# Kernel tuning notes

Measured on AMD Instinct MI355X. Metric: run time of the kernel, lower is better.

Reference implementation:

```python
import jax, jax.numpy as jnp
import numpy as np

SCALE = 32 ** (-0.5)  # hardcoded in the original module, independent of head_size

def setup_inputs() -> dict:
    key = jax.random.key(0)
    k1, k2, k3, k4 = jax.random.split(key, 4)
    B, T, E, H = 8, 4096, 2048, 128
    x = jax.random.normal(k1, (B, T, E), dtype=jnp.float32)
    Wq = jax.random.normal(k2, (E, H), dtype=jnp.float32) * (E ** -0.5)
    Wk = jax.random.normal(k3, (E, H), dtype=jnp.float32) * (E ** -0.5)
    Wv = jax.random.normal(k4, (E, H), dtype=jnp.float32) * (E ** -0.5)
    return {"x": x, "Wq": Wq, "Wk": Wk, "Wv": Wv}

def reference(x, Wq, Wk, Wv):
    # q,k,v: [B,T,H]
    q = jnp.einsum('bte,eh->bth', x, Wq)
    k = jnp.einsum('bte,eh->bth', x, Wk)
    v = jnp.einsum('bte,eh->bth', x, Wv)
    # wei: [B, T(query), T(key)]
    wei = jnp.einsum('bqh,bkh->bqk', q, k) * SCALE
    # NOTE: original uses F.softmax(wei, dim=1) -> normalize over the QUERY axis
    wei = jax.nn.softmax(wei, axis=1)
    # dropout prob is 0 in this deterministic baseline (eval mode)
    out = jnp.einsum('bqk,bkh->bqh', wei, v)
    return out
```

## Files before the change

kernel.cpp:

```cpp
#include <hip/hip_runtime.h>
#include <hip/hip_bf16.h>
#include <hip/hip_fp16.h>

#define Bn 8
#define Tn 4096
#define En 2048
#define Hn 128

typedef __attribute__((ext_vector_type(8))) short bf16x8;
typedef __attribute__((ext_vector_type(4))) float f32x4;
typedef __attribute__((ext_vector_type(4))) unsigned int u32x4;

typedef const __attribute__((address_space(1))) unsigned int* gptr_t;
typedef __attribute__((address_space(3))) unsigned int* lptr_t;

static __device__ __forceinline__ void gload16(const void* g, void* l) {
    __builtin_amdgcn_global_load_lds((gptr_t)g, (lptr_t)l, 16, 0, 0);
}

static __device__ __forceinline__ unsigned short f2bf(float f) {
    union { float f; unsigned u; } v; v.f = f;
    unsigned r = v.u + 0x7FFFu + ((v.u >> 16) & 1u);
    return (unsigned short)(r >> 16);
}

#define MFMA16(a, b, c) __builtin_amdgcn_mfma_f32_16x16x32_bf16((a), (b), (c), 0, 0, 0)
#define EXP2F(x) __builtin_amdgcn_exp2f(x)
#define WAIT_VM_PUB(N) do { asm volatile("s_waitcnt vmcnt(" #N ")" ::: "memory"); \
                            __builtin_amdgcn_sched_barrier(0); \
                            __builtin_amdgcn_s_barrier(); \
                            __builtin_amdgcn_sched_barrier(0); } while (0)
#define LGKM_BARRIER() do { asm volatile("s_waitcnt lgkmcnt(0)" ::: "memory"); \
                            __builtin_amdgcn_s_barrier(); \
                            __builtin_amdgcn_sched_barrier(0); } while (0)

__global__ __launch_bounds__(256) void conv_x(const float* __restrict__ x,
                                              unsigned short* __restrict__ xb) {
    size_t i = ((size_t)blockIdx.x * 256 + threadIdx.x) * 8;
    float4 a = *reinterpret_cast<const float4*>(x + i);
    float4 b = *reinterpret_cast<const float4*>(x + i + 4);
    ushort4 o0, o1;
    o0.x = f2bf(a.x); o0.y = f2bf(a.y); o0.z = f2bf(a.z); o0.w = f2bf(a.w);
    o1.x = f2bf(b.x); o1.y = f2bf(b.y); o1.z = f2bf(b.z); o1.w = f2bf(b.w);
    *reinterpret_cast<ushort4*>(xb + i) = o0;
    *reinterpret_cast<ushort4*>(xb + i + 4) = o1;
}

__global__ __launch_bounds__(256) void prep_w(const float* __restrict__ Wq,
                                              const float* __restrict__ Wk,
                                              const float* __restrict__ Wv,
                                              unsigned short* __restrict__ Wt) {
    int idx = blockIdx.x * 256 + threadIdx.x;
    int w = idx / (En * Hn);
    int rem = idx - w * (En * Hn);
    int kx = rem >> 7;
    int n  = rem & 127;
    const float* W = (w == 0) ? Wq : (w == 1) ? Wk : Wv;
    float f = W[rem];
    if (w == 0) f *= (0.17677669529663687f * 1.4426950408889634f);
    Wt[(size_t)w * En * Hn + (size_t)n * En + kx] = f2bf(f);
}

__global__ __launch_bounds__(256, 3) void qkv_mfma(const unsigned short* __restrict__ xb,
                                                   const unsigned short* __restrict__ Wt,
                                                   unsigned short* __restrict__ qs,
                                                   unsigned short* __restrict__ ks,
                                                   unsigned short* __restrict__ vT) {
    __shared__ unsigned short Al[128][64];
    __shared__ unsigned short Bl[128][64];
    const int bid = blockIdx.x;
    const int w = bid % 3;
    const int m0 = (bid / 3) * 128;
    const int b = m0 >> 12;
    const int tb = m0 & (Tn - 1);
    const int t = threadIdx.x;
    const int lane = t & 63, wid = t >> 6;
    const int wr = (wid >> 1) * 64, wc = (wid & 1) * 64;
    const int fr = lane & 15, fq = lane >> 4;
    const unsigned short* Wb = Wt + (size_t)w * En * Hn;
    const int sr = lane >> 3, sc = lane & 7;

    f32x4 acc[4][4] = {};
    for (int k0 = 0; k0 < En; k0 += 64) {
        __syncthreads();
        #pragma unroll
        for (int s = 0; s < 4; ++s) {
            int seg = wid * 4 + s;
            int r = seg * 8 + sr;
            gload16(&xb[(size_t)(m0 + r) * En + k0 + sc * 8],
                    (char*)&Al[0][0] + seg * 1024 + lane * 16);
            gload16(&Wb[(size_t)r * En + k0 + sc * 8],
                    (char*)&Bl[0][0] + seg * 1024 + lane * 16);
        }
        __syncthreads();
        #pragma unroll
        for (int ksub = 0; ksub < 2; ++ksub) {
            bf16x8 av[4], bv[4];
            #pragma unroll
            for (int mi = 0; mi < 4; ++mi)
                av[mi] = *reinterpret_cast<const bf16x8*>(&Al[wr + mi * 16 + fr][ksub * 32 + fq * 8]);
            #pragma unroll
            for (int ni = 0; ni < 4; ++ni)
                bv[ni] = *reinterpret_cast<const bf16x8*>(&Bl[wc + ni * 16 + fr][ksub * 32 + fq * 8]);
            #pragma unroll
            for (int mi = 0; mi < 4; ++mi)
                #pragma unroll
                for (int ni = 0; ni < 4; ++ni)
                    acc[mi][ni] = MFMA16(av[mi], bv[ni], acc[mi][ni]);
        }
    }

    if (w < 2) {
        unsigned short* out = (w == 0) ? qs : ks;
        #pragma unroll
        for (int mi = 0; mi < 4; ++mi)
            #pragma unroll
            for (int ni = 0; ni < 4; ++ni)
                #pragma unroll
                for (int r = 0; r < 4; ++r) {
                    int row = m0 + wr + mi * 16 + fq * 4 + r;
                    int col = wc + ni * 16 + fr;
                    out[(size_t)row * Hn + col] = f2bf(acc[mi][ni][r]);
                }
    } else {
        #pragma unroll
        for (int mi = 0; mi < 4; ++mi)
            #pragma unroll
            for (int ni = 0; ni < 4; ++ni)
                #pragma unroll
                for (int r = 0; r < 4; ++r) {
                    int tt = tb + wr + mi * 16 + fq * 4 + r;
                    int h  = wc + ni * 16 + fr;
                    vT[((size_t)b * Hn + h) * Tn + tt] = f2bf(acc[mi][ni][r]);
                }
    }
}

__global__ __launch_bounds__(256, 3) void stats_qk(const unsigned short* __restrict__ qs,
                                                   const unsigned short* __restrict__ ks,
                                                   float2* __restrict__ part) {
    __shared__ __align__(16) char smem[49152];
    const int bid = blockIdx.x;
    const int b = bid >> 7;
    const int kt = (bid >> 1) & 63;
    const int qh = bid & 1;
    const int k0 = kt * 64;
    const unsigned short* qb = qs + (size_t)b * Tn * Hn;
    const unsigned short* kb = ks + (size_t)b * Tn * Hn;
    const int t = threadIdx.x;
    const int lane = t & 63, wid = t >> 6;
    const int wk = wid >> 1, wq = wid & 1;
    const int fr = lane & 15, fq = lane >> 4;
    const int srow = t >> 4, schk = t & 15;

    #pragma unroll
    for (int it = 0; it < 4; ++it) {
        int r = it * 16 + srow;
        gload16(&kb[(size_t)(k0 + r) * Hn + ((schk ^ (r & 15)) * 8)],
                smem + it * 4096 + t * 16);
        gload16(&qb[(size_t)(qh * 2048 + r) * Hn + ((schk ^ (r & 15)) * 8)],
                smem + 16384 + it * 4096 + t * 16);
    }
    __syncthreads();
    bf16x8 av[2][4];
    #pragma unroll
    for (int mi = 0; mi < 2; ++mi)
        #pragma unroll
        for (int kc = 0; kc < 4; ++kc) {
            int row = wk * 32 + mi * 16 + fr;
            int ch = (kc * 4 + fq) ^ (row & 15);
            av[mi][kc] = *reinterpret_cast<const bf16x8*>(smem + row * 256 + ch * 16);
        }

    float m[2][4], l[2][4];
    #pragma unroll
    for (int mi = 0; mi < 2; ++mi)
        #pragma unroll
        for (int r = 0; r < 4; ++r) { m[mi][r] = -INFINITY; l[mi][r] = 0.f; }

    for (int step = 0; step < 32; ++step) {
        const int cur = step & 1;
        const int qn = qh * 2048 + ((step + 1) & 31) * 64;
        #pragma unroll
        for (int it = 0; it < 4; ++it) {
            int r = it * 16 + srow;
            gload16(&qb[(size_t)(qn + r) * Hn + ((schk ^ (r & 15)) * 8)],
                    smem + 16384 + (cur ^ 1) * 16384 + it * 4096 + t * 16);
        }
        WAIT_VM_PUB(4);
        const char* Qc = smem + 16384 + cur * 16384;
        f32x4 acc[2][2] = {};
        __builtin_amdgcn_s_setprio(1);
        #pragma unroll
        for (int kc = 0; kc < 4; ++kc) {
            bf16x8 bv[2];
            #pragma unroll
            for (int ni = 0; ni < 2; ++ni) {
                int row = wq * 32 + ni * 16 + fr;
                int ch = (kc * 4 + fq) ^ (row & 15);
                bv[ni] = *reinterpret_cast<const bf16x8*>(Qc + row * 256 + ch * 16);
            }
            #pragma unroll
            for (int mi = 0; mi < 2; ++mi)
                #pragma unroll
                for (int ni = 0; ni < 2; ++ni)
                    acc[mi][ni] = MFMA16(av[mi][kc], bv[ni], acc[mi][ni]);
        }
        __builtin_amdgcn_s_setprio(0);
        #pragma unroll
        for (int mi = 0; mi < 2; ++mi)
            #pragma unroll
            for (int r = 0; r < 4; ++r) {
                float v0 = acc[mi][0][r], v1 = acc[mi][1][r];
                float mn = fmaxf(m[mi][r], fmaxf(v0, v1));
                l[mi][r] = l[mi][r] * EXP2F(m[mi][r] - mn) + EXP2F(v0 - mn) + EXP2F(v1 - mn);
                m[mi][r] = mn;
            }
        LGKM_BARRIER();
    }
    #pragma unroll
    for (int off = 1; off <= 8; off <<= 1) {
        #pragma unroll
        for (int mi = 0; mi < 2; ++mi)
            #pragma unroll
            for (int r = 0; r < 4; ++r) {
                float mo = __shfl_xor(m[mi][r], off);
                float lo = __shfl_xor(l[mi][r], off);
                float mn = fmaxf(m[mi][r], mo);
                l[mi][r] = l[mi][r] * EXP2F(m[mi][r] - mn) + lo * EXP2F(mo - mn);
                m[mi][r] = mn;
            }
    }
    if (fr == 0) {
        #pragma unroll
        for (int mi = 0; mi < 2; ++mi)
            #pragma unroll
            for (int r = 0; r < 4; ++r) {
                int k = k0 + wk * 32 + mi * 16 + fq * 4 + r;
                part[((size_t)b * Tn + k) * 4 + qh * 2 + wq] = make_float2(m[mi][r], l[mi][r]);
            }
    }
}

__global__ __launch_bounds__(256) void stats_comb(const float2* __restrict__ part,
                                                  float* __restrict__ mr) {
    int g = blockIdx.x * 256 + threadIdx.x;
    const float2* pp = part + (size_t)g * 4;
    float2 p0 = pp[0], p1 = pp[1], p2 = pp[2], p3 = pp[3];
    float M = fmaxf(fmaxf(p0.x, p1.x), fmaxf(p2.x, p3.x));
    float L = p0.y * EXP2F(p0.x - M) + p1.y * EXP2F(p1.x - M) +
              p2.y * EXP2F(p2.x - M) + p3.y * EXP2F(p3.x - M);
    mr[g] = M + __log2f(L);
}

__global__ __launch_bounds__(256, 2) void attn_pv(const unsigned short* __restrict__ qs,
                                                  const unsigned short* __restrict__ ks,
                                                  const unsigned short* __restrict__ vT,
                                                  const float* __restrict__ mr,
                                                  float* __restrict__ out) {
    __shared__ __align__(16) char smem[73728];
    char* Pb = smem + 65536;
    const int bid = blockIdx.x;
    const int b = bid >> 6;
    const int q0 = (bid & 63) * 64;
    const unsigned short* qg = qs + (size_t)b * Tn * Hn;
    const unsigned short* kg = ks + (size_t)b * Tn * Hn;
    const unsigned short* vg = vT + (size_t)b * Hn * Tn;
    const float* mrb = mr + (size_t)b * Tn;
    const int t = threadIdx.x;
    const int lane = t & 63, wid = t >> 6;
    const int wk = wid >> 1, wq = wid & 1;
    const int fr = lane & 15, fq = lane >> 4;
    const int srow16 = t >> 4, schk16 = t & 15;
    const int srow8 = t >> 3, schk8 = t & 7;

    bf16x8 bq[2][4];
    #pragma unroll
    for (int ni = 0; ni < 2; ++ni)
        #pragma unroll
        for (int kc = 0; kc < 4; ++kc) {
            int row = q0 + wq * 32 + ni * 16 + fr;
            bq[ni][kc] = *reinterpret_cast<const bf16x8*>(&qg[(size_t)row * Hn + kc * 32 + fq * 8]);
        }
    #pragma unroll
    for (int it = 0; it < 4; ++it) {
        int r = it * 16 + srow16;
        gload16(&kg[(size_t)r * Hn + ((schk16 ^ (r & 15)) * 8)], smem + it * 4096 + t * 16);
        int rv = it * 32 + srow8;
        gload16(&vg[(size_t)rv * Tn + ((schk8 ^ (rv & 7)) * 8)],
                smem + 32768 + it * 4096 + t * 16);
    }
    __syncthreads();

    f32x4 acc_o[4][2] = {};
    for (int kt = 0; kt < 64; ++kt) {
        const int cur = kt & 1;
        const int k0 = kt * 64;
        float4 mk0 = *reinterpret_cast<const float4*>(&mrb[k0 + wk * 32 + fq * 4]);
        float4 mk1 = *reinterpret_cast<const float4*>(&mrb[k0 + wk * 32 + 16 + fq * 4]);
        __builtin_amdgcn_sched_barrier(0);
        {
            const int knr = ((kt + 1) & 63) * 64;
            #pragma unroll
            for (int it = 0; it < 4; ++it) {
                int r = it * 16 + srow16;
                gload16(&kg[(size_t)(knr + r) * Hn + ((schk16 ^ (r & 15)) * 8)],
                        smem + (cur ^ 1) * 16384 + it * 4096 + t * 16);
                int rv = it * 32 + srow8;
                gload16(&vg[(size_t)rv * Tn + knr + ((schk8 ^ (rv & 7)) * 8)],
                        smem + 32768 + (cur ^ 1) * 16384 + it * 4096 + t * 16);
            }
        }
        WAIT_VM_PUB(8);
        const char* Kc = smem + cur * 16384;
        f32x4 acc_s[2][2] = {};
        __builtin_amdgcn_s_setprio(1);
        #pragma unroll
        for (int kc = 0; kc < 4; ++kc) {
            bf16x8 avk[2];
            #pragma unroll
            for (int mi = 0; mi < 2; ++mi) {
                int row = wk * 32 + mi * 16 + fr;
                int ch = (kc * 4 + fq) ^ (row & 15);
                avk[mi] = *reinterpret_cast<const bf16x8*>(Kc + row * 256 + ch * 16);
            }
            #pragma unroll
            for (int mi = 0; mi < 2; ++mi)
                #pragma unroll
                for (int ni = 0; ni < 2; ++ni)
                    acc_s[mi][ni] = MFMA16(avk[mi], bq[ni][kc], acc_s[mi][ni]);
        }
        __builtin_amdgcn_s_setprio(0);
        #pragma unroll
        for (int mi = 0; mi < 2; ++mi) {
            float4 mk = mi ? mk1 : mk0;
            #pragma unroll
            for (int ni = 0; ni < 2; ++ni) {
                unsigned p01 = (unsigned)f2bf(EXP2F(acc_s[mi][ni][0] - mk.x)) |
                               ((unsigned)f2bf(EXP2F(acc_s[mi][ni][1] - mk.y)) << 16);
                unsigned p23 = (unsigned)f2bf(EXP2F(acc_s[mi][ni][2] - mk.z)) |
                               ((unsigned)f2bf(EXP2F(acc_s[mi][ni][3] - mk.w)) << 16);
                int q = wq * 32 + ni * 16 + fr;
                int chunk = (wk * 4 + mi * 2 + (fq >> 1)) ^ (q & 7);
                *reinterpret_cast<uint2*>(Pb + q * 128 + chunk * 16 + (fq & 1) * 8) =
                    make_uint2(p01, p23);
            }
        }
        LGKM_BARRIER();
        const char* Vc = smem + 32768 + cur * 16384;
        __builtin_amdgcn_s_setprio(1);
        #pragma unroll
        for (int kc = 0; kc < 2; ++kc) {
            bf16x8 bp[2];
            #pragma unroll
            for (int ni = 0; ni < 2; ++ni) {
                int qrow = wq * 32 + ni * 16 + fr;
                int ch = (kc * 4 + fq) ^ (qrow & 7);
                bp[ni] = *reinterpret_cast<const bf16x8*>(Pb + qrow * 128 + ch * 16);
            }
            #pragma unroll
            for (int mi = 0; mi < 4; ++mi) {
                int row = wk * 64 + mi * 16 + fr;
                int ch = (kc * 4 + fq) ^ (row & 7);
                bf16x8 avv = *reinterpret_cast<const bf16x8*>(Vc + row * 128 + ch * 16);
                #pragma unroll
                for (int ni = 0; ni < 2; ++ni)
                    acc_o[mi][ni] = MFMA16(avv, bp[ni], acc_o[mi][ni]);
            }
        }
        __builtin_amdgcn_s_setprio(0);
        LGKM_BARRIER();
    }

    float* Ol = (float*)smem;
    __syncthreads();
    #pragma unroll
    for (int mi = 0; mi < 4; ++mi)
        #pragma unroll
        for (int ni = 0; ni < 2; ++ni) {
            int q = wq * 32 + ni * 16 + fr;
            int h = wk * 64 + mi * 16 + fq * 4;
            *reinterpret_cast<float4*>(&Ol[q * 132 + h]) =
                make_float4(acc_o[mi][ni][0], acc_o[mi][ni][1], acc_o[mi][ni][2], acc_o[mi][ni][3]);
        }
    __syncthreads();
    #pragma unroll
    for (int j = 0; j < 8; ++j) {
        int idx = j * 256 + t;
        int row = idx >> 5, c = (idx & 31) * 4;
        *reinterpret_cast<float4*>(&out[((size_t)b * Tn + q0 + row) * Hn + c]) =
            *reinterpret_cast<const float4*>(&Ol[row * 132 + c]);
    }
}

extern "C" void kernel_launch(void* const* d_in, const int* in_sizes, int n_in,
                              void* d_out, int out_size, void* d_ws, size_t ws_size,
                              hipStream_t stream) {
    const float* x  = (const float*)d_in[0];
    const float* Wq = (const float*)d_in[1];
    const float* Wk = (const float*)d_in[2];
    const float* Wv = (const float*)d_in[3];
    float* out = (float*)d_out;

    char* p = (char*)d_ws;
    unsigned short* qs = (unsigned short*)p; p += (size_t)Bn * Tn * Hn * 2;
    unsigned short* ks = (unsigned short*)p; p += (size_t)Bn * Tn * Hn * 2;
    unsigned short* vT = (unsigned short*)p; p += (size_t)Bn * Tn * Hn * 2;
    unsigned short* Wt = (unsigned short*)p; p += (size_t)3 * En * Hn * 2;
    unsigned short* xb = (unsigned short*)p; p += (size_t)Bn * Tn * En * 2;
    float2* part       = (float2*)p;         p += (size_t)Bn * Tn * 4 * sizeof(float2);
    float* mr          = (float*)p;          p += (size_t)Bn * Tn * sizeof(float);
    size_t needed = (size_t)(p - (char*)d_ws);
    if (ws_size < needed) return;

    conv_x<<<dim3(Bn * Tn * En / (256 * 8)), dim3(256), 0, stream>>>(x, xb);
    prep_w<<<dim3(3 * En * Hn / 256), dim3(256), 0, stream>>>(Wq, Wk, Wv, Wt);
    qkv_mfma<<<dim3((Bn * Tn / 128) * 3), dim3(256), 0, stream>>>(xb, Wt, qs, ks, vT);
    stats_qk<<<dim3(Bn * 64 * 2), dim3(256), 0, stream>>>(qs, ks, part);
    stats_comb<<<dim3(Bn * Tn / 256), dim3(256), 0, stream>>>(part, mr);
    attn_pv<<<dim3(Bn * 64), dim3(256), 0, stream>>>(qs, ks, vT, mr, out);
}
```

Measured before the change: 296.1 us.

## Fuse fp32-to-bf16 conversion of x into QKV GEMM and swizzle LDS tiles

Removes the separate conv_x kernel and its bf16 copy of x. The QKV GEMM now loads fp32 x straight into XOR-swizzled LDS and converts it to bf16 with packed conversion instructions just before the MFMAs. The W tile gets an XOR swizzle as well. The stats and attention kernels change their block-to-batch mapping so batches interleave across blocks, and the exp results are packed to bf16 with the hardware instruction. The cost is that the GEMM now reads x at fp32 width three times, once per Q/K/V block, and the A tile takes double the LDS, which may hurt occupancy.

```diff
diff --git a/kernel.cpp b/kernel.cpp
--- a/kernel.cpp
+++ b/kernel.cpp
@@ -22,6 +22,11 @@
     union { float f; unsigned u; } v; v.f = f;
     unsigned r = v.u + 0x7FFFu + ((v.u >> 16) & 1u);
     return (unsigned short)(r >> 16);
+}
+static __device__ __forceinline__ unsigned cvtpk(float lo, float hi) {
+    unsigned r;
+    asm volatile("v_cvt_pk_bf16_f32 %0, %1, %2" : "=v"(r) : "v"(lo), "v"(hi));
+    return r;
 }
 
 #define MFMA16(a, b, c) __builtin_amdgcn_mfma_f32_16x16x32_bf16((a), (b), (c), 0, 0, 0)
@@ -33,18 +38,6 @@
 #define LGKM_BARRIER() do { asm volatile("s_waitcnt lgkmcnt(0)" ::: "memory"); \
                             __builtin_amdgcn_s_barrier(); \
                             __builtin_amdgcn_sched_barrier(0); } while (0)
-
-__global__ __launch_bounds__(256) void conv_x(const float* __restrict__ x,
-                                              unsigned short* __restrict__ xb) {
-    size_t i = ((size_t)blockIdx.x * 256 + threadIdx.x) * 8;
-    float4 a = *reinterpret_cast<const float4*>(x + i);
-    float4 b = *reinterpret_cast<const float4*>(x + i + 4);
-    ushort4 o0, o1;
-    o0.x = f2bf(a.x); o0.y = f2bf(a.y); o0.z = f2bf(a.z); o0.w = f2bf(a.w);
-    o1.x = f2bf(b.x); o1.y = f2bf(b.y); o1.z = f2bf(b.z); o1.w = f2bf(b.w);
-    *reinterpret_cast<ushort4*>(xb + i) = o0;
-    *reinterpret_cast<ushort4*>(xb + i + 4) = o1;
-}
 
 __global__ __launch_bounds__(256) void prep_w(const float* __restrict__ Wq,
                                               const float* __restrict__ Wk,
@@ -61,13 +54,13 @@
     Wt[(size_t)w * En * Hn + (size_t)n * En + kx] = f2bf(f);
 }
 
-__global__ __launch_bounds__(256, 3) void qkv_mfma(const unsigned short* __restrict__ xb,
+__global__ __launch_bounds__(256, 3) void qkv_mfma(const float* __restrict__ x,
                                                    const unsigned short* __restrict__ Wt,
                                                    unsigned short* __restrict__ qs,
                                                    unsigned short* __restrict__ ks,
                                                    unsigned short* __restrict__ vT) {
-    __shared__ unsigned short Al[128][64];
-    __shared__ unsigned short Bl[128][64];
+    __shared__ __align__(16) float Al[128][64];
+    __shared__ __align__(16) unsigned short Bl[128][64];
     const int bid = blockIdx.x;
     const int w = bid % 3;
     const int m0 = (bid / 3) * 128;
@@ -78,30 +71,50 @@
     const int wr = (wid >> 1) * 64, wc = (wid & 1) * 64;
     const int fr = lane & 15, fq = lane >> 4;
     const unsigned short* Wb = Wt + (size_t)w * En * Hn;
-    const int sr = lane >> 3, sc = lane & 7;
+    const int aR = lane >> 4, aC = lane & 15;
+    const int bR = lane >> 3, bC = lane & 7;
 
     f32x4 acc[4][4] = {};
     for (int k0 = 0; k0 < En; k0 += 64) {
         __syncthreads();
         #pragma unroll
+        for (int s = 0; s < 8; ++s) {
+            int seg = wid * 8 + s;
+            int r = seg * 4 + aR;
+            gload16(&x[(size_t)(m0 + r) * En + k0 + ((aC ^ (r & 15)) * 4)],
+                    (char*)Al + seg * 1024 + lane * 16);
+        }
+        #pragma unroll
         for (int s = 0; s < 4; ++s) {
             int seg = wid * 4 + s;
-            int r = seg * 8 + sr;
-            gload16(&xb[(size_t)(m0 + r) * En + k0 + sc * 8],
-                    (char*)&Al[0][0] + seg * 1024 + lane * 16);
-            gload16(&Wb[(size_t)r * En + k0 + sc * 8],
-                    (char*)&Bl[0][0] + seg * 1024 + lane * 16);
+            int r = seg * 8 + bR;
+            gload16(&Wb[(size_t)r * En + k0 + ((bC ^ (r & 7)) * 8)],
+                    (char*)Bl + seg * 1024 + lane * 16);
         }
         __syncthreads();
         #pragma unroll
         for (int ksub = 0; ksub < 2; ++ksub) {
             bf16x8 av[4], bv[4];
             #pragma unroll
-            for (int mi = 0; mi < 4; ++mi)
-                av[mi] = *reinterpret_cast<const bf16x8*>(&Al[wr + mi * 16 + fr][ksub * 32 + fq * 8]);
-            #pragma unroll
-            for (int ni = 0; ni < 4; ++ni)
-                bv[ni] = *reinterpret_cast<const bf16x8*>(&Bl[wc + ni * 16 + fr][ksub * 32 + fq * 8]);
+            for (int mi = 0; mi < 4; ++mi) {
+                int row = wr + mi * 16 + fr;
+                const char* base = (const char*)Al + row * 256;
+                int c0 = ksub * 8 + fq * 2;
+                f32x4 a0 = *(const f32x4*)(base + ((c0 ^ (row & 15)) << 4));
+                f32x4 a1 = *(const f32x4*)(base + (((c0 + 1) ^ (row & 15)) << 4));
+                u32x4 pk;
+                pk[0] = cvtpk(a0[0], a0[1]);
+                pk[1] = cvtpk(a0[2], a0[3]);
+                pk[2] = cvtpk(a1[0], a1[1]);
+                pk[3] = cvtpk(a1[2], a1[3]);
+                av[mi] = *reinterpret_cast<bf16x8*>(&pk);
+            }
+            #pragma unroll
+            for (int ni = 0; ni < 4; ++ni) {
+                int row = wc + ni * 16 + fr;
+                int ch = (ksub * 4 + fq) ^ (row & 7);
+                bv[ni] = *reinterpret_cast<const bf16x8*>((const char*)Bl + row * 128 + ch * 16);
+            }
             #pragma unroll
             for (int mi = 0; mi < 4; ++mi)
                 #pragma unroll
@@ -141,9 +154,10 @@
                                                    float2* __restrict__ part) {
     __shared__ __align__(16) char smem[49152];
     const int bid = blockIdx.x;
-    const int b = bid >> 7;
-    const int kt = (bid >> 1) & 63;
-    const int qh = bid & 1;
+    const int b = bid & 7;
+    const int rest = bid >> 3;
+    const int kt = rest & 63;
+    const int qh = rest >> 6;
     const int k0 = kt * 64;
     const unsigned short* qb = qs + (size_t)b * Tn * Hn;
     const unsigned short* kb = ks + (size_t)b * Tn * Hn;
@@ -261,8 +275,8 @@
     __shared__ __align__(16) char smem[73728];
     char* Pb = smem + 65536;
     const int bid = blockIdx.x;
-    const int b = bid >> 6;
-    const int q0 = (bid & 63) * 64;
+    const int b = bid & 7;
+    const int q0 = (bid >> 3) * 64;
     const unsigned short* qg = qs + (size_t)b * Tn * Hn;
     const unsigned short* kg = ks + (size_t)b * Tn * Hn;
     const unsigned short* vg = vT + (size_t)b * Hn * Tn;
@@ -336,14 +350,14 @@
             float4 mk = mi ? mk1 : mk0;
             #pragma unroll
             for (int ni = 0; ni < 2; ++ni) {
-                unsigned p01 = (unsigned)f2bf(EXP2F(acc_s[mi][ni][0] - mk.x)) |
-                               ((unsigned)f2bf(EXP2F(acc_s[mi][ni][1] - mk.y)) << 16);
-                unsigned p23 = (unsigned)f2bf(EXP2F(acc_s[mi][ni][2] - mk.z)) |
-                               ((unsigned)f2bf(EXP2F(acc_s[mi][ni][3] - mk.w)) << 16);
+                float e0 = EXP2F(acc_s[mi][ni][0] - mk.x);
+                float e1 = EXP2F(acc_s[mi][ni][1] - mk.y);
+                float e2 = EXP2F(acc_s[mi][ni][2] - mk.z);
+                float e3 = EXP2F(acc_s[mi][ni][3] - mk.w);
                 int q = wq * 32 + ni * 16 + fr;
                 int chunk = (wk * 4 + mi * 2 + (fq >> 1)) ^ (q & 7);
                 *reinterpret_cast<uint2*>(Pb + q * 128 + chunk * 16 + (fq & 1) * 8) =
-                    make_uint2(p01, p23);
+                    make_uint2(cvtpk(e0, e1), cvtpk(e2, e3));
             }
         }
         LGKM_BARRIER();
@@ -407,15 +421,13 @@
     unsigned short* ks = (unsigned short*)p; p += (size_t)Bn * Tn * Hn * 2;
     unsigned short* vT = (unsigned short*)p; p += (size_t)Bn * Tn * Hn * 2;
     unsigned short* Wt = (unsigned short*)p; p += (size_t)3 * En * Hn * 2;
-    unsigned short* xb = (unsigned short*)p; p += (size_t)Bn * Tn * En * 2;
     float2* part       = (float2*)p;         p += (size_t)Bn * Tn * 4 * sizeof(float2);
     float* mr          = (float*)p;          p += (size_t)Bn * Tn * sizeof(float);
     size_t needed = (size_t)(p - (char*)d_ws);
     if (ws_size < needed) return;
 
-    conv_x<<<dim3(Bn * Tn * En / (256 * 8)), dim3(256), 0, stream>>>(x, xb);
     prep_w<<<dim3(3 * En * Hn / 256), dim3(256), 0, stream>>>(Wq, Wk, Wv, Wt);
-    qkv_mfma<<<dim3((Bn * Tn / 128) * 3), dim3(256), 0, stream>>>(xb, Wt, qs, ks, vT);
+    qkv_mfma<<<dim3((Bn * Tn / 128) * 3), dim3(256), 0, stream>>>(x, Wt, qs, ks, vT);
     stats_qk<<<dim3(Bn * 64 * 2), dim3(256), 0, stream>>>(qs, ks, part);
     stats_comb<<<dim3(Bn * Tn / 256), dim3(256), 0, stream>>>(part, mr);
     attn_pv<<<dim3(Bn * 64), dim3(256), 0, stream>>>(qs, ks, vT, mr, out);
```

New measurement: 276.2 us. 1.07x faster.
